# Optimization experiments

Hardware: AMD Instinct MI355X
Metric: run time of the kernel (lower is better)

The kernel has to match this reference:

```python
import jax, jax.numpy as jnp
import numpy as np

NUM_CHANNELS = 512
B_DIM = 64
C_DIM = 16
N = 512
FEAT = NUM_CHANNELS * 4 * 4  # 8192


def setup_inputs() -> dict:
    key = jax.random.key(0)
    k1, k2 = jax.random.split(key)
    inp = jax.random.normal(k1, (N, NUM_CHANNELS, 4, 4), dtype=jnp.float32)
    T = jax.random.normal(k2, (FEAT, B_DIM * C_DIM), dtype=jnp.float32) * 0.1
    return {"inp": inp, "T": T}


def reference(inp, T):
    x = inp.reshape(-1, FEAT)                      # (N, 8192)
    M = (x @ T).reshape(-1, B_DIM, C_DIM)          # (N, B, C)
    # pairwise L1 distance over C: (N, N, B)
    dist = jnp.sum(jnp.abs(M[:, None, :, :] - M[None, :, :, :]), axis=-1)
    o = jnp.sum(jnp.exp(-dist), axis=1)            # (N, B)
    return jnp.concatenate((x, o), axis=1)         # (N, 8192 + B)
```

## Files before the change

### kernel.cpp

```cpp
#include <hip/hip_runtime.h>

#define NROWS 512
#define FEAT  8192
#define BDIM  64
#define CDIM  16
#define MCOLS 1024
#define OUTC  8256
#define KSPLIT 8
#define KCHUNK (FEAT / KSPLIT)
#define KSTEPS (KCHUNK / 64)
#define MSIZE  (NROWS * MCOLS)

typedef __bf16 bf16x8 __attribute__((ext_vector_type(8)));
typedef float  floatx4 __attribute__((ext_vector_type(4)));

static __device__ __forceinline__ unsigned int pk2(float a, float b) {
    unsigned short lo = __builtin_bit_cast(unsigned short, (__bf16)a);
    unsigned short hi = __builtin_bit_cast(unsigned short, (__bf16)b);
    return (unsigned int)lo | ((unsigned int)hi << 16);
}

__global__ __launch_bounds__(512, 2) void k_gemm(const float* __restrict__ x,
                                                 const float* __restrict__ T,
                                                 float* __restrict__ Mp,
                                                 float* __restrict__ out) {
    __shared__ __align__(16) unsigned short ldsA[2][128 * 64];
    __shared__ __align__(16) unsigned short ldsB[2][128 * 64];
    char* ldsAc = (char*)ldsA;
    char* ldsBc = (char*)ldsB;

    int bid = blockIdx.x;
    int wg = (bid & 7) * 32 + (bid >> 3);
    int mt = wg & 3, nt = (wg >> 2) & 7, ks = wg >> 5;
    int m0 = mt * 128, n0 = nt * 128, kbase = ks * KCHUNK;
    int t = threadIdx.x, w = t >> 6, l = t & 63;
    bool docopy = (nt == ks);

    int arow = t >> 4, aq = t & 15;
    const float* gA = x + (size_t)(m0 + arow) * FEAT + kbase + aq * 4;
    float* gC = out + (size_t)(m0 + arow) * OUTC + kbase + aq * 4;
    int swa = (arow & 7) ^ ((arow >> 2) & 7);
    int wA = arow * 128 + (((aq >> 1) ^ swa) << 4) + ((aq & 1) << 3);

    int n4 = t & 31, kg = t >> 5;
    const float* gB = T + (size_t)(kbase + kg * 4) * MCOLS + n0 + n4 * 4;
    int wB0, wB1, wB2, wB3;
    {
        int n_0 = n4 * 4 + 0, n_1 = n4 * 4 + 1, n_2 = n4 * 4 + 2, n_3 = n4 * 4 + 3;
        wB0 = n_0 * 128 + (((kg >> 1) ^ ((n_0 & 7) ^ ((n_0 >> 2) & 7))) << 4) + ((kg & 1) << 3);
        wB1 = n_1 * 128 + (((kg >> 1) ^ ((n_1 & 7) ^ ((n_1 >> 2) & 7))) << 4) + ((kg & 1) << 3);
        wB2 = n_2 * 128 + (((kg >> 1) ^ ((n_2 & 7) ^ ((n_2 >> 2) & 7))) << 4) + ((kg & 1) << 3);
        wB3 = n_3 * 128 + (((kg >> 1) ^ ((n_3 & 7) ^ ((n_3 >> 2) & 7))) << 4) + ((kg & 1) << 3);
    }

    int wr = w >> 2, wc = w & 3, fm = l & 15, fq = l >> 4;
    int swf = (fm & 7) ^ ((fm >> 2) & 7);
    int baseA = (wr * 64 + fm) * 128 + ((fq ^ swf) << 4);
    int baseB = (wc * 32 + fm) * 128 + ((fq ^ swf) << 4);

    floatx4 acc[4][2] = {};

    float4 va00, va01, va02, va03, vb00, vb01, vb02, vb03;
    float4 va10, va11, va12, va13, vb10, vb11, vb12, vb13;

#define ISSUE(A0, A1, A2, A3, B0, B1, B2, B3, KK) do {                      \
        const float* pa_ = gA + (KK) * 64;                                  \
        A0 = *(const float4*)(pa_);                                         \
        A1 = *(const float4*)(pa_ + 32 * FEAT);                             \
        A2 = *(const float4*)(pa_ + 64 * FEAT);                             \
        A3 = *(const float4*)(pa_ + 96 * FEAT);                             \
        const float* pb_ = gB + (size_t)(KK) * 64 * MCOLS;                  \
        B0 = *(const float4*)(pb_);                                         \
        B1 = *(const float4*)(pb_ + MCOLS);                                 \
        B2 = *(const float4*)(pb_ + 2 * MCOLS);                             \
        B3 = *(const float4*)(pb_ + 3 * MCOLS);                             \
    } while (0)

#define WRITE(A0, A1, A2, A3, B0, B1, B2, B3, SO, KK) do {                  \
        uint2 u_;                                                           \
        u_.x = pk2(A0.x, A0.y); u_.y = pk2(A0.z, A0.w);                     \
        *(uint2*)(ldsAc + (SO) + wA + 0 * 4096) = u_;                       \
        u_.x = pk2(A1.x, A1.y); u_.y = pk2(A1.z, A1.w);                     \
        *(uint2*)(ldsAc + (SO) + wA + 1 * 4096) = u_;                       \
        u_.x = pk2(A2.x, A2.y); u_.y = pk2(A2.z, A2.w);                     \
        *(uint2*)(ldsAc + (SO) + wA + 2 * 4096) = u_;                       \
        u_.x = pk2(A3.x, A3.y); u_.y = pk2(A3.z, A3.w);                     \
        *(uint2*)(ldsAc + (SO) + wA + 3 * 4096) = u_;                       \
        u_.x = pk2(B0.x, B1.x); u_.y = pk2(B2.x, B3.x);                     \
        *(uint2*)(ldsBc + (SO) + wB0) = u_;                                 \
        u_.x = pk2(B0.y, B1.y); u_.y = pk2(B2.y, B3.y);                     \
        *(uint2*)(ldsBc + (SO) + wB1) = u_;                                 \
        u_.x = pk2(B0.z, B1.z); u_.y = pk2(B2.z, B3.z);                     \
        *(uint2*)(ldsBc + (SO) + wB2) = u_;                                 \
        u_.x = pk2(B0.w, B1.w); u_.y = pk2(B2.w, B3.w);                     \
        *(uint2*)(ldsBc + (SO) + wB3) = u_;                                 \
        if (docopy) {                                                       \
            *(float4*)(gC + (size_t)0 * 32 * OUTC + (KK) * 64) = A0;        \
            *(float4*)(gC + (size_t)1 * 32 * OUTC + (KK) * 64) = A1;        \
            *(float4*)(gC + (size_t)2 * 32 * OUTC + (KK) * 64) = A2;        \
            *(float4*)(gC + (size_t)3 * 32 * OUTC + (KK) * 64) = A3;        \
        }                                                                   \
    } while (0)

#define MFMA_PHASE(SO) do {                                                 \
        _Pragma("unroll")                                                   \
        for (int h = 0; h < 2; ++h) {                                       \
            bf16x8 af[4], bfr[2];                                           \
            _Pragma("unroll")                                               \
            for (int a = 0; a < 4; ++a)                                     \
                af[a] = *(const bf16x8*)(ldsAc + (SO) + ((baseA + a * 2048) ^ ((h ^ (a & 1)) << 6))); \
            _Pragma("unroll")                                               \
            for (int b = 0; b < 2; ++b)                                     \
                bfr[b] = *(const bf16x8*)(ldsBc + (SO) + ((baseB + b * 2048) ^ ((h ^ (b & 1)) << 6))); \
            _Pragma("unroll")                                               \
            for (int a = 0; a < 4; ++a)                                     \
                _Pragma("unroll")                                           \
                for (int b = 0; b < 2; ++b)                                 \
                    acc[a][b] = __builtin_amdgcn_mfma_f32_16x16x32_bf16(af[a], bfr[b], acc[a][b], 0, 0, 0); \
        }                                                                   \
    } while (0)

    ISSUE(va00, va01, va02, va03, vb00, vb01, vb02, vb03, 0);
    ISSUE(va10, va11, va12, va13, vb10, vb11, vb12, vb13, 1);
    for (int kk = 0; kk < KSTEPS; kk += 2) {
        WRITE(va00, va01, va02, va03, vb00, vb01, vb02, vb03, 0, kk);
        if (kk + 2 < KSTEPS)
            ISSUE(va00, va01, va02, va03, vb00, vb01, vb02, vb03, kk + 2);
        asm volatile("s_waitcnt lgkmcnt(0)" ::: "memory");
        __builtin_amdgcn_sched_barrier(0);
        __builtin_amdgcn_s_barrier();
        MFMA_PHASE(0);
        WRITE(va10, va11, va12, va13, vb10, vb11, vb12, vb13, 16384, kk + 1);
        if (kk + 3 < KSTEPS)
            ISSUE(va10, va11, va12, va13, vb10, vb11, vb12, vb13, kk + 3);
        asm volatile("s_waitcnt lgkmcnt(0)" ::: "memory");
        __builtin_amdgcn_sched_barrier(0);
        __builtin_amdgcn_s_barrier();
        MFMA_PHASE(16384);
    }
#undef ISSUE
#undef WRITE
#undef MFMA_PHASE

    float* outp = Mp + (size_t)ks * MSIZE;
    int gr0 = m0 + wr * 64, gc0 = n0 + wc * 32;
#pragma unroll
    for (int a = 0; a < 4; ++a)
#pragma unroll
        for (int r = 0; r < 4; ++r) {
            int row = gr0 + a * 16 + fq * 4 + r;
#pragma unroll
            for (int b = 0; b < 2; ++b)
                outp[(size_t)row * MCOLS + gc0 + b * 16 + fm] = acc[a][b][r];
        }
}

__global__ __launch_bounds__(512, 1) void k_pair(const float* __restrict__ Mp,
                                                 float* __restrict__ out) {
    __shared__ __align__(16) float ldsM[NROWS * 20];
    __shared__ float partial[8][64];
    int bid = blockIdx.x, t = threadIdx.x;
    int b = bid & 63, itp = bid >> 6;

#pragma unroll
    for (int p = 0; p < 4; ++p) {
        int idx = t + p * 512;
        int j = idx >> 2, c4 = idx & 3;
        const float* base = Mp + (size_t)j * MCOLS + b * CDIM + c4 * 4;
        float4 s = *(const float4*)base;
#pragma unroll
        for (int k = 1; k < KSPLIT; ++k) {
            float4 v = *(const float4*)(base + (size_t)k * MSIZE);
            s.x += v.x; s.y += v.y; s.z += v.z; s.w += v.w;
        }
        *(float4*)&ldsM[j * 20 + c4 * 4] = s;
    }
    __syncthreads();

    int lane = t & 63, w = t >> 6, g = t >> 8, wg = (t >> 6) & 3;
    int i = (itp * 2 + g) * 64 + lane;
    float4 mi0 = *(const float4*)&ldsM[i * 20 + 0];
    float4 mi1 = *(const float4*)&ldsM[i * 20 + 4];
    float4 mi2 = *(const float4*)&ldsM[i * 20 + 8];
    float4 mi3 = *(const float4*)&ldsM[i * 20 + 12];

    float acc = 0.0f;
    for (int jj = wg * 128; jj < wg * 128 + 128; ++jj) {
        const float4* rp = (const float4*)&ldsM[jj * 20];
        float4 a0 = rp[0], a1 = rp[1], a2 = rp[2], a3 = rp[3];
        float d = fabsf(mi0.x - a0.x) + fabsf(mi0.y - a0.y)
                + fabsf(mi0.z - a0.z) + fabsf(mi0.w - a0.w)
                + fabsf(mi1.x - a1.x) + fabsf(mi1.y - a1.y)
                + fabsf(mi1.z - a1.z) + fabsf(mi1.w - a1.w)
                + fabsf(mi2.x - a2.x) + fabsf(mi2.y - a2.y)
                + fabsf(mi2.z - a2.z) + fabsf(mi2.w - a2.w)
                + fabsf(mi3.x - a3.x) + fabsf(mi3.y - a3.y)
                + fabsf(mi3.z - a3.z) + fabsf(mi3.w - a3.w);
        acc += __expf(-d);
    }
    partial[w][lane] = acc;
    __syncthreads();
    if ((t & 255) < 64) {
        int ii = (itp * 2 + g) * 64 + (t & 63);
        float o = partial[g * 4 + 0][t & 63] + partial[g * 4 + 1][t & 63] +
                  partial[g * 4 + 2][t & 63] + partial[g * 4 + 3][t & 63];
        out[(size_t)ii * OUTC + FEAT + b] = o;
    }
}

extern "C" void kernel_launch(void* const* d_in, const int* in_sizes, int n_in,
                              void* d_out, int out_size, void* d_ws, size_t ws_size,
                              hipStream_t stream) {
    const float* x = (const float*)d_in[0];
    const float* T = (const float*)d_in[1];
    float* out = (float*)d_out;

    float* Mp = (float*)d_ws;

    k_gemm<<<256, 512, 0, stream>>>(x, T, Mp, out);
    k_pair<<<256, 512, 0, stream>>>(Mp, out);
}
```

Before: 130.4 us.

## Halve GEMM M-tile to 64 rows and double workgroup count

The GEMM tile shrinks from 128x128 to 64x128, so the kernel now launches 512 workgroups instead of 256, and launch bounds rise to allow 4 blocks per CU. The global-load prefetch drops from two register stages to one, which lowers register pressure and LDS use so more workgroups can be resident. The aim is better CU occupancy and latency hiding on a grid that previously left many CUs underused. In exchange, B tiles are loaded twice as often across blocks, and each MFMA phase does less work per LDS load.

```diff
diff --git a/kernel.cpp b/kernel.cpp
--- a/kernel.cpp
+++ b/kernel.cpp
@@ -20,27 +20,28 @@
     return (unsigned int)lo | ((unsigned int)hi << 16);
 }
 
-__global__ __launch_bounds__(512, 2) void k_gemm(const float* __restrict__ x,
+__global__ __launch_bounds__(512, 4) void k_gemm(const float* __restrict__ x,
                                                  const float* __restrict__ T,
                                                  float* __restrict__ Mp,
                                                  float* __restrict__ out) {
-    __shared__ __align__(16) unsigned short ldsA[2][128 * 64];
+    __shared__ __align__(16) unsigned short ldsA[2][64 * 64];
     __shared__ __align__(16) unsigned short ldsB[2][128 * 64];
     char* ldsAc = (char*)ldsA;
     char* ldsBc = (char*)ldsB;
 
     int bid = blockIdx.x;
-    int wg = (bid & 7) * 32 + (bid >> 3);
-    int mt = wg & 3, nt = (wg >> 2) & 7, ks = wg >> 5;
-    int m0 = mt * 128, n0 = nt * 128, kbase = ks * KCHUNK;
+    int wg = (bid & 7) * 64 + (bid >> 3);
+    int mt = wg & 7, nt = (wg >> 3) & 7, ks = wg >> 6;
+    int m0 = mt * 64, n0 = nt * 128, kbase = ks * KCHUNK;
     int t = threadIdx.x, w = t >> 6, l = t & 63;
     bool docopy = (nt == ks);
 
-    int arow = t >> 4, aq = t & 15;
-    const float* gA = x + (size_t)(m0 + arow) * FEAT + kbase + aq * 4;
-    float* gC = out + (size_t)(m0 + arow) * OUTC + kbase + aq * 4;
+    int arow = t >> 3, aq2 = t & 7;
+    const float* gA = x + (size_t)(m0 + arow) * FEAT + kbase + aq2 * 4;
+    float* gC = out + (size_t)(m0 + arow) * OUTC + kbase + aq2 * 4;
     int swa = (arow & 7) ^ ((arow >> 2) & 7);
-    int wA = arow * 128 + (((aq >> 1) ^ swa) << 4) + ((aq & 1) << 3);
+    int wA0 = arow * 128 + (((aq2 >> 1) ^ swa) << 4) + ((aq2 & 1) << 3);
+    int wA1 = wA0 ^ 64;
 
     int n4 = t & 31, kg = t >> 5;
     const float* gB = T + (size_t)(kbase + kg * 4) * MCOLS + n0 + n4 * 4;
@@ -55,97 +56,84 @@
 
     int wr = w >> 2, wc = w & 3, fm = l & 15, fq = l >> 4;
     int swf = (fm & 7) ^ ((fm >> 2) & 7);
-    int baseA = (wr * 64 + fm) * 128 + ((fq ^ swf) << 4);
+    int baseA = (wr * 32 + fm) * 128 + ((fq ^ swf) << 4);
     int baseB = (wc * 32 + fm) * 128 + ((fq ^ swf) << 4);
 
-    floatx4 acc[4][2] = {};
-
-    float4 va00, va01, va02, va03, vb00, vb01, vb02, vb03;
-    float4 va10, va11, va12, va13, vb10, vb11, vb12, vb13;
-
-#define ISSUE(A0, A1, A2, A3, B0, B1, B2, B3, KK) do {                      \
+    floatx4 acc[2][2] = {};
+    float4 va0, va1, vb0, vb1, vb2, vb3;
+
+#define ISSUE(KK) do {                                                      \
         const float* pa_ = gA + (KK) * 64;                                  \
-        A0 = *(const float4*)(pa_);                                         \
-        A1 = *(const float4*)(pa_ + 32 * FEAT);                             \
-        A2 = *(const float4*)(pa_ + 64 * FEAT);                             \
-        A3 = *(const float4*)(pa_ + 96 * FEAT);                             \
+        va0 = *(const float4*)(pa_);                                        \
+        va1 = *(const float4*)(pa_ + 32);                                   \
         const float* pb_ = gB + (size_t)(KK) * 64 * MCOLS;                  \
-        B0 = *(const float4*)(pb_);                                         \
-        B1 = *(const float4*)(pb_ + MCOLS);                                 \
-        B2 = *(const float4*)(pb_ + 2 * MCOLS);                             \
-        B3 = *(const float4*)(pb_ + 3 * MCOLS);                             \
+        vb0 = *(const float4*)(pb_);                                        \
+        vb1 = *(const float4*)(pb_ + MCOLS);                                \
+        vb2 = *(const float4*)(pb_ + 2 * MCOLS);                            \
+        vb3 = *(const float4*)(pb_ + 3 * MCOLS);                            \
     } while (0)
 
-#define WRITE(A0, A1, A2, A3, B0, B1, B2, B3, SO, KK) do {                  \
+#define WRITE(SOA, SOB, KK) do {                                            \
         uint2 u_;                                                           \
-        u_.x = pk2(A0.x, A0.y); u_.y = pk2(A0.z, A0.w);                     \
-        *(uint2*)(ldsAc + (SO) + wA + 0 * 4096) = u_;                       \
-        u_.x = pk2(A1.x, A1.y); u_.y = pk2(A1.z, A1.w);                     \
-        *(uint2*)(ldsAc + (SO) + wA + 1 * 4096) = u_;                       \
-        u_.x = pk2(A2.x, A2.y); u_.y = pk2(A2.z, A2.w);                     \
-        *(uint2*)(ldsAc + (SO) + wA + 2 * 4096) = u_;                       \
-        u_.x = pk2(A3.x, A3.y); u_.y = pk2(A3.z, A3.w);                     \
-        *(uint2*)(ldsAc + (SO) + wA + 3 * 4096) = u_;                       \
-        u_.x = pk2(B0.x, B1.x); u_.y = pk2(B2.x, B3.x);                     \
-        *(uint2*)(ldsBc + (SO) + wB0) = u_;                                 \
-        u_.x = pk2(B0.y, B1.y); u_.y = pk2(B2.y, B3.y);                     \
-        *(uint2*)(ldsBc + (SO) + wB1) = u_;                                 \
-        u_.x = pk2(B0.z, B1.z); u_.y = pk2(B2.z, B3.z);                     \
-        *(uint2*)(ldsBc + (SO) + wB2) = u_;                                 \
-        u_.x = pk2(B0.w, B1.w); u_.y = pk2(B2.w, B3.w);                     \
-        *(uint2*)(ldsBc + (SO) + wB3) = u_;                                 \
+        u_.x = pk2(va0.x, va0.y); u_.y = pk2(va0.z, va0.w);                 \
+        *(uint2*)(ldsAc + (SOA) + wA0) = u_;                                \
+        u_.x = pk2(va1.x, va1.y); u_.y = pk2(va1.z, va1.w);                 \
+        *(uint2*)(ldsAc + (SOA) + wA1) = u_;                                \
+        u_.x = pk2(vb0.x, vb1.x); u_.y = pk2(vb2.x, vb3.x);                 \
+        *(uint2*)(ldsBc + (SOB) + wB0) = u_;                                \
+        u_.x = pk2(vb0.y, vb1.y); u_.y = pk2(vb2.y, vb3.y);                 \
+        *(uint2*)(ldsBc + (SOB) + wB1) = u_;                                \
+        u_.x = pk2(vb0.z, vb1.z); u_.y = pk2(vb2.z, vb3.z);                 \
+        *(uint2*)(ldsBc + (SOB) + wB2) = u_;                                \
+        u_.x = pk2(vb0.w, vb1.w); u_.y = pk2(vb2.w, vb3.w);                 \
+        *(uint2*)(ldsBc + (SOB) + wB3) = u_;                                \
         if (docopy) {                                                       \
-            *(float4*)(gC + (size_t)0 * 32 * OUTC + (KK) * 64) = A0;        \
-            *(float4*)(gC + (size_t)1 * 32 * OUTC + (KK) * 64) = A1;        \
-            *(float4*)(gC + (size_t)2 * 32 * OUTC + (KK) * 64) = A2;        \
-            *(float4*)(gC + (size_t)3 * 32 * OUTC + (KK) * 64) = A3;        \
+            *(float4*)(gC + (KK) * 64) = va0;                               \
+            *(float4*)(gC + (KK) * 64 + 32) = va1;                          \
         }                                                                   \
     } while (0)
 
-#define MFMA_PHASE(SO) do {                                                 \
+#define MFMA_PHASE(SOA, SOB) do {                                           \
         _Pragma("unroll")                                                   \
         for (int h = 0; h < 2; ++h) {                                       \
-            bf16x8 af[4], bfr[2];                                           \
+            bf16x8 af[2], bfr[2];                                           \
             _Pragma("unroll")                                               \
-            for (int a = 0; a < 4; ++a)                                     \
-                af[a] = *(const bf16x8*)(ldsAc + (SO) + ((baseA + a * 2048) ^ ((h ^ (a & 1)) << 6))); \
+            for (int a = 0; a < 2; ++a)                                     \
+                af[a] = *(const bf16x8*)(ldsAc + (SOA) + ((baseA + a * 2048) ^ ((h ^ a) << 6))); \
             _Pragma("unroll")                                               \
             for (int b = 0; b < 2; ++b)                                     \
-                bfr[b] = *(const bf16x8*)(ldsBc + (SO) + ((baseB + b * 2048) ^ ((h ^ (b & 1)) << 6))); \
+                bfr[b] = *(const bf16x8*)(ldsBc + (SOB) + ((baseB + b * 2048) ^ ((h ^ b) << 6))); \
             _Pragma("unroll")                                               \
-            for (int a = 0; a < 4; ++a)                                     \
+            for (int a = 0; a < 2; ++a)                                     \
                 _Pragma("unroll")                                           \
                 for (int b = 0; b < 2; ++b)                                 \
                     acc[a][b] = __builtin_amdgcn_mfma_f32_16x16x32_bf16(af[a], bfr[b], acc[a][b], 0, 0, 0); \
         }                                                                   \
     } while (0)
 
-    ISSUE(va00, va01, va02, va03, vb00, vb01, vb02, vb03, 0);
-    ISSUE(va10, va11, va12, va13, vb10, vb11, vb12, vb13, 1);
+    ISSUE(0);
     for (int kk = 0; kk < KSTEPS; kk += 2) {
-        WRITE(va00, va01, va02, va03, vb00, vb01, vb02, vb03, 0, kk);
-        if (kk + 2 < KSTEPS)
-            ISSUE(va00, va01, va02, va03, vb00, vb01, vb02, vb03, kk + 2);
+        WRITE(0, 0, kk);
+        ISSUE(kk + 1);
         asm volatile("s_waitcnt lgkmcnt(0)" ::: "memory");
         __builtin_amdgcn_sched_barrier(0);
         __builtin_amdgcn_s_barrier();
-        MFMA_PHASE(0);
-        WRITE(va10, va11, va12, va13, vb10, vb11, vb12, vb13, 16384, kk + 1);
-        if (kk + 3 < KSTEPS)
-            ISSUE(va10, va11, va12, va13, vb10, vb11, vb12, vb13, kk + 3);
+        MFMA_PHASE(0, 0);
+        WRITE(8192, 16384, kk + 1);
+        if (kk + 2 < KSTEPS) ISSUE(kk + 2);
         asm volatile("s_waitcnt lgkmcnt(0)" ::: "memory");
         __builtin_amdgcn_sched_barrier(0);
         __builtin_amdgcn_s_barrier();
-        MFMA_PHASE(16384);
+        MFMA_PHASE(8192, 16384);
     }
 #undef ISSUE
 #undef WRITE
 #undef MFMA_PHASE
 
     float* outp = Mp + (size_t)ks * MSIZE;
-    int gr0 = m0 + wr * 64, gc0 = n0 + wc * 32;
-#pragma unroll
-    for (int a = 0; a < 4; ++a)
+    int gr0 = m0 + wr * 32, gc0 = n0 + wc * 32;
+#pragma unroll
+    for (int a = 0; a < 2; ++a)
 #pragma unroll
         for (int r = 0; r < 4; ++r) {
             int row = gr0 + a * 16 + fq * 4 + r;
@@ -217,6 +205,6 @@
 
     float* Mp = (float*)d_ws;
 
-    k_gemm<<<256, 512, 0, stream>>>(x, T, Mp, out);
+    k_gemm<<<512, 512, 0, stream>>>(x, T, Mp, out);
     k_pair<<<256, 512, 0, stream>>>(Mp, out);
 }
```

New measurement: 141.6 us. 8.6% more time.
